# Optimization experiments

Measured on AMD Instinct MI355X. Metric: run time of the kernel, lower is better.

The kernel has to match this reference:

```python
import jax, jax.numpy as jnp
import numpy as np

N = 100000       # num nodes
E = 1600000      # num edges
D_IN = 32
D_HID = 32
D_OUT = 32
K = 3            # Chebyshev order (number of terms)


def setup_inputs() -> dict:
    key = jax.random.key(0)
    k1, k2, k3, k4, k5, k6 = jax.random.split(key, 6)
    x = jax.random.normal(k1, (N, D_IN), dtype=jnp.float32)
    edge_index = jax.random.randint(k2, (2, E), 0, N, dtype=jnp.int64)
    s1 = 1.0 / np.sqrt(D_IN)
    s2 = 1.0 / np.sqrt(D_HID)
    W1 = jax.random.uniform(k3, (K, D_IN, D_HID), jnp.float32, -s1, s1)
    b1 = jax.random.uniform(k4, (D_HID,), jnp.float32, -s1, s1)
    W2 = jax.random.uniform(k5, (K, D_HID, D_OUT), jnp.float32, -s2, s2)
    b2 = jax.random.uniform(k6, (D_OUT,), jnp.float32, -s2, s2)
    return {"x": x, "edge_index": edge_index, "W1": W1, "b1": b1, "W2": W2, "b2": b2}


def _prop(x, row, col, w):
    # L_hat @ x : gather along col, scale by edge weight, scatter-add to row.
    # (diagonal of the rescaled Laplacian cancels to 0 in PyG ChebConv with
    #  sym normalization and lambda_max=2, so only off-diagonal edges remain)
    return jax.ops.segment_sum(w[:, None] * x[col], row, num_segments=N)


def _cheb_conv(x, row, col, w, W, b):
    # Chebyshev recurrence: Tx0 = x, Tx1 = L_hat x, Tx_k = 2 L_hat Tx_{k-1} - Tx_{k-2}
    k_terms = W.shape[0]
    Tx0 = x
    out = Tx0 @ W[0]
    if k_terms > 1:
        Tx1 = _prop(Tx0, row, col, w)
        out = out + Tx1 @ W[1]
        for k in range(2, k_terms):
            Tx2 = 2.0 * _prop(Tx1, row, col, w) - Tx0
            out = out + Tx2 @ W[k]
            Tx0, Tx1 = Tx1, Tx2
    return out + b


def reference(x, edge_index, W1, b1, W2, b2):
    row, col = edge_index[0], edge_index[1]
    mask = (row != col).astype(x.dtype)            # remove_self_loops
    deg = jax.ops.segment_sum(mask, row, num_segments=N)
    dinv = jnp.where(deg > 0, 1.0 / jnp.sqrt(jnp.maximum(deg, 1.0)), 0.0)
    w = -mask * dinv[row] * dinv[col]              # scaled Laplacian off-diagonal weights
    x0 = x
    h = jax.nn.relu(_cheb_conv(x, row, col, w, W1, b1))
    h = _cheb_conv(h, row, col, w, W2, b2)
    return h + x0
```

## Files before the change

### kernel.cpp

```cpp
#include <hip/hip_runtime.h>

#define NN 100000
#define EE 1600000
#define DD 32
#define NBUK 391
#define BROWS 256
#define TILE 4096
#define NT 391
#define BCAP2 4864

#define TOTP   106176
#define ENT2SZ 2084352

__constant__ int c_cap[9]   = {0, 2944, 56320, 43520, 2944, 256, 64, 64, 64};
__constant__ int c_pbase[9] = {0, 0, 2944, 59264, 102784, 105728, 105984, 106048, 106112};
__constant__ int c_ebase[9] = {0, 0, 23552, 924672, 1969152, 2063360, 2073600, 2076672, 2080256};

typedef unsigned int uint;
typedef unsigned short ushort;
typedef unsigned char uchar;
typedef __attribute__((ext_vector_type(8))) short bf16x8;
typedef __attribute__((ext_vector_type(4))) float f32x4;
typedef __attribute__((ext_vector_type(2))) float f32x2;

typedef __attribute__((ext_vector_type(4))) uint u32x4v;
typedef __attribute__((ext_vector_type(2))) uint u32x2v;
typedef __attribute__((ext_vector_type(4))) int i32x4v;
typedef __attribute__((ext_vector_type(4))) float f32x4v;

__device__ __forceinline__ uint4 ntld(const uint4* p) {
    u32x4v v = __builtin_nontemporal_load((const u32x4v*)p);
    uint4 r; r.x = v.x; r.y = v.y; r.z = v.z; r.w = v.w; return r;
}
__device__ __forceinline__ uint2 ntld(const uint2* p) {
    u32x2v v = __builtin_nontemporal_load((const u32x2v*)p);
    uint2 r; r.x = v.x; r.y = v.y; return r;
}
__device__ __forceinline__ int4 ntld(const int4* p) {
    i32x4v v = __builtin_nontemporal_load((const i32x4v*)p);
    int4 r; r.x = v.x; r.y = v.y; r.z = v.z; r.w = v.w; return r;
}
__device__ __forceinline__ float4 ntld(const float4* p) {
    f32x4v v = __builtin_nontemporal_load((const f32x4v*)p);
    float4 r; r.x = v.x; r.y = v.y; r.z = v.z; r.w = v.w; return r;
}
__device__ __forceinline__ int   ntld(const int* p)   { return __builtin_nontemporal_load(p); }
__device__ __forceinline__ float ntld(const float* p) { return __builtin_nontemporal_load(p); }
__device__ __forceinline__ void ntst(uint4* p, uint4 v) {
    u32x4v w; w.x = v.x; w.y = v.y; w.z = v.z; w.w = v.w;
    __builtin_nontemporal_store(w, (u32x4v*)p);
}
__device__ __forceinline__ void ntst(int4* p, int4 v) {
    uint4 u; u.x = (uint)v.x; u.y = (uint)v.y; u.z = (uint)v.z; u.w = (uint)v.w;
    ntst((uint4*)p, u);
}
__device__ __forceinline__ void ntst(uint2* p, uint2 v) {
    u32x2v w; w.x = v.x; w.y = v.y;
    __builtin_nontemporal_store(w, (u32x2v*)p);
}
__device__ __forceinline__ void ntst(int* p, int v)     { __builtin_nontemporal_store(v, p); }
__device__ __forceinline__ void ntst(float* p, float v) { __builtin_nontemporal_store(v, p); }

__device__ __forceinline__ ushort f2b(float f) {
    uint u = __float_as_uint(f);
    u += 0x7fffu + ((u >> 16) & 1u);
    return (ushort)(u >> 16);
}
__device__ __forceinline__ uint f2e4(float f) {
    uint u = __float_as_uint(f);
    uint s = (u >> 24) & 0x80u;
    float a = fabsf(f) * 0x1p-120f;
    uint g = __float_as_uint(a);
    g += 0x7FFFFu + ((g >> 20) & 1u);
    uint m = g >> 20;
    if (m > 0x7Eu) m = 0x7Eu;
    return s | m;
}
__device__ __forceinline__ bf16x8 as_bf16x8(uint4 v) {
    union { uint4 u; bf16x8 b; } cv; cv.u = v; return cv.b;
}
__device__ __forceinline__ void acc8(float* acc, uint2 v) {
#pragma unroll
    for (int wi = 0; wi < 2; ++wi) {
        uint w = (&v.x)[wi];
        f32x2 lo = __builtin_amdgcn_cvt_pk_f32_fp8((int)w, false);
        f32x2 hi = __builtin_amdgcn_cvt_pk_f32_fp8((int)w, true);
        acc[wi * 4 + 0] += lo.x;
        acc[wi * 4 + 1] += lo.y;
        acc[wi * 4 + 2] += hi.x;
        acc[wi * 4 + 3] += hi.y;
    }
}


__global__ void k_part(const int* __restrict__ ei, int* __restrict__ gtail,
                       int* __restrict__ pairs) {
    __shared__ int hist[512];
    __shared__ int gbase[512];
    int t = threadIdx.x;
    hist[t] = 0; hist[t + 256] = 0;
    __syncthreads();
    int e0 = blockIdx.x * TILE;
    int pk[16], rk[16], bb[16];
#pragma unroll
    for (int k = 0; k < 16; ++k) {
        int e = e0 + t + k * 256;
        bb[k] = -1;
        if (e < EE) {
            int r = ntld(ei + e), c = ntld(ei + EE + e);
            if (r != c) {
                bb[k] = r >> 8;
                pk[k] = (r & (BROWS - 1)) | (c << 8);
                rk[k] = atomicAdd(&hist[bb[k]], 1);
            }
        }
    }
    __syncthreads();
    for (int q = t; q < NBUK; q += 256) {
        int cnt = hist[q];
        gbase[q] = cnt ? atomicAdd(&gtail[q * 16], cnt) : 0;
    }
    __syncthreads();
#pragma unroll
    for (int k = 0; k < 16; ++k) {
        if (bb[k] >= 0) {
            int pos = gbase[bb[k]] + rk[k];
            if (pos < BCAP2) pairs[bb[k] * BCAP2 + pos] = pk[k];
        }
    }
}


__global__ void k_build2(const int* __restrict__ gtail, const int* __restrict__ pairs,
                         float* __restrict__ dinv, int* __restrict__ ctail,
                         int* __restrict__ ent2, int4* __restrict__ pdesc) {
    __shared__ int lcnt[BROWS];
    __shared__ int lh[16];
    __shared__ int gb[16];
    __shared__ int sofs[BROWS];
    __shared__ uchar scls[BROWS];
    __shared__ int slab[BROWS * 64];
    int b = blockIdx.x, t = threadIdx.x;
    lcnt[t] = 0;
    if (t < 16) lh[t] = 0;
    for (int i = t; i < BROWS * 64; i += 256) slab[i] = NN;
    __syncthreads();
    int cnt = gtail[b * 16]; if (cnt > BCAP2) cnt = BCAP2;
    const int* pp = pairs + b * BCAP2;
    for (int i = t; i < cnt; i += 256) {
        int v = ntld(pp + i);
        int lr = v & (BROWS - 1);
        int pos = atomicAdd(&lcnt[lr], 1);
        if (pos < 64) slab[(lr << 6) + pos] = (int)((uint)v >> 8);
    }
    __syncthreads();
    int n = b * BROWS + t;
    int cpl = 0, lrank = 0;
    float dv = 0.0f;
    if (n < NN) {
        int d = lcnt[t];
        int ms = d > 64 ? 64 : d;
        int cls = (ms + 7) >> 3;
        cpl = cls ? cls : 1;
        dv = d > 0 ? rsqrtf((float)d) : 0.0f;
        dinv[n] = dv;
        lrank = atomicAdd(&lh[cpl], 1);
    }
    __syncthreads();
    if (t < 16) gb[t] = lh[t] ? atomicAdd(&ctail[t], lh[t]) : 0;
    __syncthreads();
    int myofs = -1;
    if (n < NN) {
        int rank = gb[cpl] + lrank;
        if (rank < c_cap[cpl]) {
            myofs = c_ebase[cpl] + rank * (cpl << 3);
            int4 pv; pv.x = n; pv.y = cpl; pv.z = (int)__float_as_uint(dv); pv.w = 0;
            pdesc[c_pbase[cpl] + rank] = pv;
        }
    }
    sofs[t] = myofs;
    scls[t] = (uchar)cpl;
    __syncthreads();
    for (int i = t; i < BROWS * 16; i += 256) {
        int row = i >> 4, piece = i & 15;
        int ofs = sofs[row];
        if (ofs >= 0 && piece < (scls[row] << 1)) {
            int4 v = *(const int4*)&slab[(row << 6) + (piece << 2)];
            ntst((int4*)&ent2[ofs + (piece << 2)], v);
        }
    }
}


__global__ void k_cvt(const float* __restrict__ x, uint2* __restrict__ xb,
                      uint* __restrict__ xb8, const float* __restrict__ dinv,
                      const float* __restrict__ W1, const float* __restrict__ W2,
                      ushort* __restrict__ wb1, ushort* __restrict__ wb2,
                      uint* __restrict__ t1b8, uint* __restrict__ hb8) {
    if (blockIdx.x == (NN * DD / 4) / 256) {
        for (int i = threadIdx.x; i < 6144; i += 256) {
            const float* W = W1; ushort* wb = wb1;
            int ii = i;
            if (ii >= 3072) { ii -= 3072; W = W2; wb = wb2; }
            int term = ii >> 10, rem = ii & 1023;
            int h = rem >> 9, lane = (rem >> 3) & 63, j = rem & 7;
            int k = ((lane >> 4) << 3) + j;
            int col = (h << 4) | (lane & 15);
            float val = W[term * 1024 + k * 32 + col];
            if (term == 0) val -= W[2 * 1024 + k * 32 + col];
            wb[ii] = f2b(val);
        }
        return;
    }
    if (blockIdx.x == 0) {
        if (threadIdx.x >= 64 && threadIdx.x < 72) xb8[NN * 8 + threadIdx.x - 64] = 0;
        if (threadIdx.x >= 72 && threadIdx.x < 80) t1b8[NN * 8 + threadIdx.x - 72] = 0;
        if (threadIdx.x >= 80 && threadIdx.x < 88) hb8[NN * 8 + threadIdx.x - 80] = 0;
    }
    int tid = blockIdx.x * blockDim.x + threadIdx.x;
    if (tid >= NN * DD / 4) return;
    float4 v = ntld(((const float4*)x) + tid);
    uint2 b;
    b.x = (uint)f2b(v.x) | ((uint)f2b(v.y) << 16);
    b.y = (uint)f2b(v.z) | ((uint)f2b(v.w) << 16);
    ntst(xb + tid, b);
    float dv = dinv[tid >> 3];
    xb8[tid] = f2e4(dv * v.x) | (f2e4(dv * v.y) << 8)
             | (f2e4(dv * v.z) << 16) | (f2e4(dv * v.w) << 24);
}


__global__ void k_prop(const int4* __restrict__ pdesc, const int* __restrict__ ent2,
                       const uint2* __restrict__ src8d,
                       uint2* __restrict__ dst8d,
                       uint4* __restrict__ dstbq,
                       float alpha) {
    int tid = blockIdx.x * blockDim.x + threadIdx.x;
    int g = tid >> 3;
    int sub = tid & 3, h = (tid >> 2) & 1;
    int4 pd = ntld(pdesc + g);
    constexpr int kPB[9] = {0, 0, 2944, 59264, 102784, 105728, 105984, 106048, 106112};
    constexpr int kEB[9] = {0, 0, 23552, 924672, 1969152, 2063360, 2073600, 2076672, 2080256};
    int cls = 1, pb = 0, eb = 0;
#pragma unroll
    for (int c = 2; c <= 8; ++c)
        if (g >= kPB[c]) { cls = c; pb = kPB[c]; eb = kEB[c]; }
    const int* ep = ent2 + eb + (g - pb) * (cls << 3);
    int mr = cls << 3;
    float acc[8] = {0, 0, 0, 0, 0, 0, 0, 0};
    for (int i = h * 8; i < mr; i += 16) {
        uint4 C0 = ntld((const uint4*)(ep + i));
        uint4 C1 = ntld((const uint4*)(ep + i + 4));
        uint2 v0 = src8d[(C0.x << 2) + sub];
        uint2 v1 = src8d[(C0.y << 2) + sub];
        uint2 v2 = src8d[(C0.z << 2) + sub];
        uint2 v3 = src8d[(C0.w << 2) + sub];
        uint2 v4 = src8d[(C1.x << 2) + sub];
        uint2 v5 = src8d[(C1.y << 2) + sub];
        uint2 v6 = src8d[(C1.z << 2) + sub];
        uint2 v7 = src8d[(C1.w << 2) + sub];
        acc8(acc, v0); acc8(acc, v1); acc8(acc, v2); acc8(acc, v3);
        acc8(acc, v4); acc8(acc, v5); acc8(acc, v6); acc8(acc, v7);
    }
    if (pd.y == 0) return;
    int n = pd.x;
    float dn = __uint_as_float((uint)pd.z);
    float s = -alpha * dn;
#pragma unroll
    for (int k = 0; k < 8; ++k)
        acc[k] = s * (acc[k] + __shfl_xor(acc[k], 4, 64));
    if (h == 0) {
        uint4 ob;
#pragma unroll
        for (int wi = 0; wi < 4; ++wi)
            (&ob.x)[wi] = (uint)f2b(acc[wi * 2]) | ((uint)f2b(acc[wi * 2 + 1]) << 16);
        ntst(dstbq + (n << 2) + sub, ob);
    } else if (dst8d) {
        uint2 o8;
        o8.x = f2e4(dn * acc[0]) | (f2e4(dn * acc[1]) << 8)
             | (f2e4(dn * acc[2]) << 16) | (f2e4(dn * acc[3]) << 24);
        o8.y = f2e4(dn * acc[4]) | (f2e4(dn * acc[5]) << 8)
             | (f2e4(dn * acc[6]) << 16) | (f2e4(dn * acc[7]) << 24);
        ntst(dst8d + (n << 2) + sub, o8);
    }
}


__global__ void k_comb(const uint4* __restrict__ t0, const uint4* __restrict__ t1,
                       const uint4* __restrict__ t2, const ushort* __restrict__ wb,
                       const float* __restrict__ bias, const float* __restrict__ residf,
                       const float* __restrict__ dinv,
                       float* __restrict__ outf, ushort* __restrict__ outb,
                       uchar* __restrict__ outb8, int do_relu) {
    int lane = threadIdx.x & 63;
    int wid = threadIdx.x >> 6;
    int n0 = (blockIdx.x * 4 + wid) << 6;
    if (n0 >= NN) return;
    int q = lane >> 4, lr = lane & 15;
    const uint4* wq = (const uint4*)wb;
    bf16x8 bf[3][2];
#pragma unroll
    for (int t = 0; t < 3; ++t)
#pragma unroll
        for (int h = 0; h < 2; ++h)
            bf[t][h] = as_bf16x8(wq[((t * 2 + h) << 6) + lane]);
    float bias0 = bias[lr], bias1 = bias[16 + lr];
    uint4 z; z.x = 0; z.y = 0; z.z = 0; z.w = 0;
#pragma unroll
    for (int mt = 0; mt < 4; ++mt) {
        int nb = n0 + (mt << 4);
        int row = nb + lr;
        bool ok = row < NN;
        int ai = (row << 2) + q;
        bf16x8 a0 = as_bf16x8(ok ? ntld((const uint4*)t0 + ai) : z);
        bf16x8 a1 = as_bf16x8(ok ? ntld((const uint4*)t1 + ai) : z);
        bf16x8 a2 = as_bf16x8(ok ? ntld((const uint4*)t2 + ai) : z);
        f32x4 c0 = {0.f, 0.f, 0.f, 0.f};
        f32x4 c1 = {0.f, 0.f, 0.f, 0.f};
        c0 = __builtin_amdgcn_mfma_f32_16x16x32_bf16(a0, bf[0][0], c0, 0, 0, 0);
        c0 = __builtin_amdgcn_mfma_f32_16x16x32_bf16(a1, bf[1][0], c0, 0, 0, 0);
        c0 = __builtin_amdgcn_mfma_f32_16x16x32_bf16(a2, bf[2][0], c0, 0, 0, 0);
        c1 = __builtin_amdgcn_mfma_f32_16x16x32_bf16(a0, bf[0][1], c1, 0, 0, 0);
        c1 = __builtin_amdgcn_mfma_f32_16x16x32_bf16(a1, bf[1][1], c1, 0, 0, 0);
        c1 = __builtin_amdgcn_mfma_f32_16x16x32_bf16(a2, bf[2][1], c1, 0, 0, 0);
#pragma unroll
        for (int r = 0; r < 4; ++r) {
            int node = nb + (q << 2) + r;
            if (node >= NN) continue;
            float v0 = c0[r] + bias0;
            float v1 = c1[r] + bias1;
            if (do_relu) { v0 = fmaxf(v0, 0.0f); v1 = fmaxf(v1, 0.0f); }
            if (outb) {
                float dv = dinv[node];
                outb[node * DD + lr] = f2b(v0);
                outb[node * DD + 16 + lr] = f2b(v1);
                outb8[node * DD + lr] = (uchar)f2e4(dv * v0);
                outb8[node * DD + 16 + lr] = (uchar)f2e4(dv * v1);
            } else {
                ntst(outf + node * DD + lr, v0 + ntld(residf + node * DD + lr));
                ntst(outf + node * DD + 16 + lr, v1 + ntld(residf + node * DD + 16 + lr));
            }
        }
    }
}


extern "C" void kernel_launch(void* const* d_in, const int* in_sizes, int n_in,
                              void* d_out, int out_size, void* d_ws, size_t ws_size,
                              hipStream_t stream) {
    const float* x  = (const float*)d_in[0];
    const int*   ei = (const int*)d_in[1];
    const float* W1 = (const float*)d_in[2];
    const float* b1 = (const float*)d_in[3];
    const float* W2 = (const float*)d_in[4];
    const float* b2 = (const float*)d_in[5];
    float* out = (float*)d_out;

    char* wsp = (char*)d_ws;
    size_t off = 0;
    auto take = [&](size_t bytes) {
        char* p = wsp + off;
        off = (off + bytes + 255) & ~(size_t)255;
        return p;
    };
    int*    ctrl  = (int*)take((size_t)(NBUK * 16 + 16) * 4);
    int*    gtail = ctrl;
    int*    ctail = ctrl + NBUK * 16;
    int4*   pdesc = (int4*)take((size_t)TOTP * 16);
    int*    ent2  = (int*)take((size_t)ENT2SZ * 4);
    float*  dinv  = (float*)take((size_t)NN * 4);
    ushort* wb1   = (ushort*)take((size_t)3072 * 2);
    ushort* wb2   = (ushort*)take((size_t)3072 * 2);
    int*    pairs = (int*)take((size_t)NBUK * BCAP2 * 4);
    ushort* xb    = (ushort*)take((size_t)NN * DD * 2);
    ushort* t1b   = (ushort*)take((size_t)NN * DD * 2);
    ushort* t2b   = (ushort*)take((size_t)NN * DD * 2);
    ushort* hb    = (ushort*)take((size_t)NN * DD * 2);
    uchar*  xb8   = (uchar*)take((size_t)(NN + 1) * DD);
    uchar*  t1b8  = (uchar*)take((size_t)(NN + 1) * DD);
    uchar*  hb8   = (uchar*)take((size_t)(NN + 1) * DD);

    size_t msz = (size_t)((char*)ent2 - (char*)ctrl) + (size_t)ENT2SZ * 4;
    hipMemsetAsync(ctrl, 0, msz, stream);

    k_part  <<<NT, 256, 0, stream>>>(ei, gtail, pairs);
    k_build2<<<NBUK, 256, 0, stream>>>(gtail, pairs, dinv, ctail, ent2, pdesc);
    k_cvt   <<<NN * DD / 4 / 256 + 1, 256, 0, stream>>>(x, (uint2*)xb, (uint*)xb8, dinv,
                                                        W1, W2, wb1, wb2,
                                                        (uint*)t1b8, (uint*)hb8);

    const int pgrid = TOTP * 8 / 256;
    const int mgrid = (NN + 255) / 256;
    k_prop<<<pgrid, 256, 0, stream>>>(pdesc, ent2, (const uint2*)xb8,
                                      (uint2*)t1b8, (uint4*)t1b, 1.0f);
    k_prop<<<pgrid, 256, 0, stream>>>(pdesc, ent2, (const uint2*)t1b8,
                                      nullptr, (uint4*)t2b, 2.0f);
    k_comb<<<mgrid, 256, 0, stream>>>((const uint4*)xb, (const uint4*)t1b,
                                      (const uint4*)t2b, wb1, b1, nullptr, dinv,
                                      nullptr, hb, hb8, 1);
    k_prop<<<pgrid, 256, 0, stream>>>(pdesc, ent2, (const uint2*)hb8,
                                      (uint2*)t1b8, (uint4*)t1b, 1.0f);
    k_prop<<<pgrid, 256, 0, stream>>>(pdesc, ent2, (const uint2*)t1b8,
                                      nullptr, (uint4*)t2b, 2.0f);
    k_comb<<<mgrid, 256, 0, stream>>>((const uint4*)hb, (const uint4*)t1b,
                                      (const uint4*)t2b, wb2, b2, x, dinv,
                                      out, nullptr, nullptr, 0);
}
```

Baseline: 233.7 us.

## Fuse input conversion into build kernel and move large memset into partition kernel

Removes the separate k_cvt launch by having each k_build2 block convert its own 256 rows of x to bf16 and scaled fp8, using dinv values kept in shared memory. An extra block handles the weight repacking and the zero padding rows. The large hipMemsetAsync over pdesc and ent2 is shrunk to cover only the control counters, and k_part blocks now zero pdesc/ent2 with streaming stores before partitioning. This saves a launch, a memset pass and a dinv reload, but puts extra store traffic into k_part and x traffic into k_build2, whose blocks already use about 70KB of shared memory.

```diff
diff --git a/kernel.cpp b/kernel.cpp
--- a/kernel.cpp
+++ b/kernel.cpp
@@ -11,6 +11,8 @@
 
 #define TOTP   106176
 #define ENT2SZ 2084352
+#define ZTOT   ((TOTP * 16 + ENT2SZ * 4) / 16)
+#define ZPB    ((ZTOT + NT - 1) / NT)
 
 __constant__ int c_cap[9]   = {0, 2944, 56320, 43520, 2944, 256, 64, 64, 64};
 __constant__ int c_pbase[9] = {0, 0, 2944, 59264, 102784, 105728, 105984, 106048, 106112};
@@ -94,7 +96,13 @@
 
 
 __global__ void k_part(const int* __restrict__ ei, int* __restrict__ gtail,
-                       int* __restrict__ pairs) {
+                       int* __restrict__ pairs, uint4* __restrict__ zbase) {
+    {
+        int z0 = blockIdx.x * ZPB;
+        int ze = z0 + ZPB; if (ze > ZTOT) ze = ZTOT;
+        uint4 zz; zz.x = 0; zz.y = 0; zz.z = 0; zz.w = 0;
+        for (int i = z0 + threadIdx.x; i < ze; i += 256) ntst(zbase + i, zz);
+    }
     __shared__ int hist[512];
     __shared__ int gbase[512];
     int t = threadIdx.x;
@@ -133,11 +141,35 @@
 
 __global__ void k_build2(const int* __restrict__ gtail, const int* __restrict__ pairs,
                          float* __restrict__ dinv, int* __restrict__ ctail,
-                         int* __restrict__ ent2, int4* __restrict__ pdesc) {
+                         int* __restrict__ ent2, int4* __restrict__ pdesc,
+                         const float* __restrict__ x, uint2* __restrict__ xb,
+                         uint* __restrict__ xb8,
+                         const float* __restrict__ W1, const float* __restrict__ W2,
+                         ushort* __restrict__ wb1, ushort* __restrict__ wb2,
+                         uint* __restrict__ t1b8, uint* __restrict__ hb8) {
+    if (blockIdx.x == NBUK) {
+        for (int i = threadIdx.x; i < 6144; i += 256) {
+            const float* W = W1; ushort* wb = wb1;
+            int ii = i;
+            if (ii >= 3072) { ii -= 3072; W = W2; wb = wb2; }
+            int term = ii >> 10, rem = ii & 1023;
+            int h = rem >> 9, lane = (rem >> 3) & 63, j = rem & 7;
+            int k = ((lane >> 4) << 3) + j;
+            int col = (h << 4) | (lane & 15);
+            float val = W[term * 1024 + k * 32 + col];
+            if (term == 0) val -= W[2 * 1024 + k * 32 + col];
+            wb[ii] = f2b(val);
+        }
+        if (threadIdx.x >= 64 && threadIdx.x < 72) xb8[NN * 8 + threadIdx.x - 64] = 0;
+        if (threadIdx.x >= 72 && threadIdx.x < 80) t1b8[NN * 8 + threadIdx.x - 72] = 0;
+        if (threadIdx.x >= 80 && threadIdx.x < 88) hb8[NN * 8 + threadIdx.x - 80] = 0;
+        return;
+    }
     __shared__ int lcnt[BROWS];
     __shared__ int lh[16];
     __shared__ int gb[16];
     __shared__ int sofs[BROWS];
+    __shared__ float sdinv[BROWS];
     __shared__ uchar scls[BROWS];
     __shared__ int slab[BROWS * 64];
     int b = blockIdx.x, t = threadIdx.x;
@@ -166,6 +198,7 @@
         dinv[n] = dv;
         lrank = atomicAdd(&lh[cpl], 1);
     }
+    sdinv[t] = dv;
     __syncthreads();
     if (t < 16) gb[t] = lh[t] ? atomicAdd(&ctail[t], lh[t]) : 0;
     __syncthreads();
@@ -189,44 +222,20 @@
             ntst((int4*)&ent2[ofs + (piece << 2)], v);
         }
     }
-}
-
-
-__global__ void k_cvt(const float* __restrict__ x, uint2* __restrict__ xb,
-                      uint* __restrict__ xb8, const float* __restrict__ dinv,
-                      const float* __restrict__ W1, const float* __restrict__ W2,
-                      ushort* __restrict__ wb1, ushort* __restrict__ wb2,
-                      uint* __restrict__ t1b8, uint* __restrict__ hb8) {
-    if (blockIdx.x == (NN * DD / 4) / 256) {
-        for (int i = threadIdx.x; i < 6144; i += 256) {
-            const float* W = W1; ushort* wb = wb1;
-            int ii = i;
-            if (ii >= 3072) { ii -= 3072; W = W2; wb = wb2; }
-            int term = ii >> 10, rem = ii & 1023;
-            int h = rem >> 9, lane = (rem >> 3) & 63, j = rem & 7;
-            int k = ((lane >> 4) << 3) + j;
-            int col = (h << 4) | (lane & 15);
-            float val = W[term * 1024 + k * 32 + col];
-            if (term == 0) val -= W[2 * 1024 + k * 32 + col];
-            wb[ii] = f2b(val);
-        }
-        return;
-    }
-    if (blockIdx.x == 0) {
-        if (threadIdx.x >= 64 && threadIdx.x < 72) xb8[NN * 8 + threadIdx.x - 64] = 0;
-        if (threadIdx.x >= 72 && threadIdx.x < 80) t1b8[NN * 8 + threadIdx.x - 72] = 0;
-        if (threadIdx.x >= 80 && threadIdx.x < 88) hb8[NN * 8 + threadIdx.x - 80] = 0;
-    }
-    int tid = blockIdx.x * blockDim.x + threadIdx.x;
-    if (tid >= NN * DD / 4) return;
-    float4 v = ntld(((const float4*)x) + tid);
-    uint2 b;
-    b.x = (uint)f2b(v.x) | ((uint)f2b(v.y) << 16);
-    b.y = (uint)f2b(v.z) | ((uint)f2b(v.w) << 16);
-    ntst(xb + tid, b);
-    float dv = dinv[tid >> 3];
-    xb8[tid] = f2e4(dv * v.x) | (f2e4(dv * v.y) << 8)
-             | (f2e4(dv * v.z) << 16) | (f2e4(dv * v.w) << 24);
+    int base4 = b * 2048;
+    for (int i = t; i < 2048; i += 256) {
+        int row = i >> 3;
+        if (b * BROWS + row < NN) {
+            float4 v = ntld((const float4*)x + base4 + i);
+            uint2 b2;
+            b2.x = (uint)f2b(v.x) | ((uint)f2b(v.y) << 16);
+            b2.y = (uint)f2b(v.z) | ((uint)f2b(v.w) << 16);
+            ntst(xb + base4 + i, b2);
+            float dvr = sdinv[row];
+            xb8[base4 + i] = f2e4(dvr * v.x) | (f2e4(dvr * v.y) << 8)
+                           | (f2e4(dvr * v.z) << 16) | (f2e4(dvr * v.w) << 24);
+        }
+    }
 }
 
 
@@ -380,14 +389,13 @@
     uchar*  t1b8  = (uchar*)take((size_t)(NN + 1) * DD);
     uchar*  hb8   = (uchar*)take((size_t)(NN + 1) * DD);
 
-    size_t msz = (size_t)((char*)ent2 - (char*)ctrl) + (size_t)ENT2SZ * 4;
-    hipMemsetAsync(ctrl, 0, msz, stream);
-
-    k_part  <<<NT, 256, 0, stream>>>(ei, gtail, pairs);
-    k_build2<<<NBUK, 256, 0, stream>>>(gtail, pairs, dinv, ctail, ent2, pdesc);
-    k_cvt   <<<NN * DD / 4 / 256 + 1, 256, 0, stream>>>(x, (uint2*)xb, (uint*)xb8, dinv,
-                                                        W1, W2, wb1, wb2,
-                                                        (uint*)t1b8, (uint*)hb8);
+    hipMemsetAsync(ctrl, 0, (size_t)(NBUK * 16 + 16) * 4, stream);
+
+    k_part  <<<NT, 256, 0, stream>>>(ei, gtail, pairs, (uint4*)pdesc);
+    k_build2<<<NBUK + 1, 256, 0, stream>>>(gtail, pairs, dinv, ctail, ent2, pdesc,
+                                           x, (uint2*)xb, (uint*)xb8,
+                                           W1, W2, wb1, wb2,
+                                           (uint*)t1b8, (uint*)hb8);
 
     const int pgrid = TOTP * 8 / 256;
     const int mgrid = (NN + 255) / 256;
```

Result: no change. 230.1 us (-1.5%).
